# Kernel optimization log

Hardware: AMD Instinct MI355X
Metric: run time of the kernel (lower is better)

Reference implementation:

```python
import jax, jax.numpy as jnp
import numpy as np

N_NODES = 100000
N_EDGES = 1600000
F_IN = 256
HID = 256
N_CLS = 40


def _glorot(key, shape):
    lim = float(np.sqrt(6.0 / (shape[0] + shape[1])))
    return jax.random.uniform(key, shape, jnp.float32, -lim, lim)


def setup_inputs() -> dict:
    key = jax.random.key(0)
    ks = jax.random.split(key, 8)
    x = jax.random.normal(ks[0], (N_NODES, F_IN), jnp.float32)
    edge_index = jax.random.randint(ks[1], (2, N_EDGES), 0, N_NODES, jnp.int64)
    return {
        "x": x,
        "edge_index": edge_index,
        "W1": _glorot(ks[2], (F_IN, HID)),
        "b1": jnp.zeros((HID,), jnp.float32),
        "W2": _glorot(ks[3], (HID, HID)),
        "b2": jnp.zeros((HID,), jnp.float32),
        "W3": _glorot(ks[4], (HID, N_CLS)),
        "b3": jnp.zeros((N_CLS,), jnp.float32),
    }


def _gcn_conv(x, W, b, src, dst, norm, num_nodes):
    # linear transform first (PyG GCNConv), then normalized scatter-add
    h = x @ W                                   # [N, out]
    msg = h[src] * norm[:, None]                # [E+N, out] gathered messages
    out = jax.ops.segment_sum(msg, dst, num_segments=num_nodes)
    return out + b


def reference(x, edge_index, W1, b1, W2, b2, W3, b3):
    n = x.shape[0]
    loop = jnp.arange(n, dtype=edge_index.dtype)
    src = jnp.concatenate([edge_index[0], loop])  # add self-loops
    dst = jnp.concatenate([edge_index[1], loop])
    # symmetric GCN normalization: deg^{-1/2}[src] * deg^{-1/2}[dst]
    deg = jax.ops.segment_sum(jnp.ones_like(dst, dtype=x.dtype), dst, num_segments=n)
    dinv = jnp.where(deg > 0, jax.lax.rsqrt(deg), 0.0)
    norm = dinv[src] * dinv[dst]

    h = jax.nn.relu(_gcn_conv(x, W1, b1, src, dst, norm, n))  # dropout p=0.0 is identity
    h = jax.nn.relu(_gcn_conv(h, W2, b2, src, dst, norm, n))
    out = _gcn_conv(h, W3, b3, src, dst, norm, n)             # logits [N, num_classes]
    return out
```

## Files before the change

kernel.cpp:

```cpp
#include <hip/hip_runtime.h>
#include <hip/hip_bf16.h>
#include <cstdint>
#include <cstddef>

#define NNODES 100000
#define NEDGES 1600000
#define NCLS 40
#define NBLK_SCAN 391
#define NBUCK 391
#define BCAP 5120
#define NBLKB 256
#define CHUNK 6250
#define MPAD 100096

typedef _Float16 f16;
typedef _Float16 f16x8 __attribute__((ext_vector_type(8)));
typedef float f32x4 __attribute__((ext_vector_type(4)));

__device__ inline float h2f(unsigned short u) {
    f16 h; __builtin_memcpy(&h, &u, 2); return (float)h;
}
__device__ inline unsigned short f2h(float f) {
    f16 h = (f16)f; unsigned short u; __builtin_memcpy(&u, &h, 2); return u;
}
__device__ inline void gload_lds16(const void* g, void* l) {
    __builtin_amdgcn_global_load_lds((const __attribute__((address_space(1))) unsigned int*)g,
                                     (__attribute__((address_space(3))) unsigned int*)l, 16, 0, 0);
}
__device__ inline void fmix2(float& alo, float& ahi, unsigned u, float one) {
    asm("v_fma_mix_f32 %0, %1, %2, %0 op_sel:[0,0,0] op_sel_hi:[1,0,0]"
        : "+v"(alo) : "v"(u), "v"(one));
    asm("v_fma_mix_f32 %0, %1, %2, %0 op_sel:[1,0,0] op_sel_hi:[1,0,0]"
        : "+v"(ahi) : "v"(u), "v"(one));
}

__global__ void k_detect(const int* __restrict__ ei, int* __restrict__ flag) {
    if (threadIdx.x == 0 && blockIdx.x == 0) {
        int nz = 0;
        for (int i = 1; i < 256; i += 2) nz |= ei[i];
        *flag = (nz == 0) ? 1 : 0;
    }
}

__global__ __launch_bounds__(256) void k_bucket(const int* __restrict__ ei,
        const int* __restrict__ flag, int* __restrict__ gbcnt, int2* __restrict__ bedge) {
    __shared__ int lcnt[NBUCK], lbase[NBUCK], lcur[NBUCK];
    const int t = threadIdx.x;
    const int is64 = *flag;
    for (int i = t; i < NBUCK; i += 256) lcnt[i] = 0;
    __syncthreads();
    const int e0 = blockIdx.x * CHUNK;
    for (int i = t; i < CHUNK; i += 256) {
        int e = e0 + i;
        int d = is64 ? ei[2 * ((size_t)NEDGES + e)] : ei[NEDGES + e];
        atomicAdd(&lcnt[d >> 8], 1);
    }
    __syncthreads();
    for (int i = t; i < NBUCK; i += 256) {
        int c = lcnt[i];
        lbase[i] = c ? atomicAdd(&gbcnt[i], c) : 0;
        lcur[i] = 0;
    }
    __syncthreads();
    for (int i = t; i < CHUNK; i += 256) {
        int e = e0 + i;
        int s, d;
        if (is64) { s = ei[2 * (size_t)e]; d = ei[2 * ((size_t)NEDGES + e)]; }
        else      { s = ei[e];             d = ei[NEDGES + e]; }
        int b = d >> 8;
        int p = lbase[b] + atomicAdd(&lcur[b], 1);
        if (p < BCAP) bedge[(size_t)b * BCAP + p] = make_int2(s, d);
    }
}

__global__ __launch_bounds__(256) void k_cnt(const int* __restrict__ gbcnt,
        const int2* __restrict__ bedge, int* __restrict__ cnt) {
    __shared__ int lc[256];
    const int t = threadIdx.x, b = blockIdx.x;
    lc[t] = 0;
    __syncthreads();
    const int ne = min(gbcnt[b], BCAP);
    const int2* be = bedge + (size_t)b * BCAP;
    for (int i = t; i < ne; i += 256)
        atomicAdd(&lc[be[i].y & 255], 1);
    __syncthreads();
    int node = b * 256 + t;
    if (node < NNODES) cnt[node] = lc[t];
}

__global__ __launch_bounds__(256) void k_dinv(const int* __restrict__ cnt, float* __restrict__ dinv) {
    int i = blockIdx.x * 256 + threadIdx.x;
    if (i < MPAD) dinv[i] = (i < NNODES) ? rsqrtf((float)(cnt[i] + 1)) : 0.f;
}

__global__ __launch_bounds__(256) void k_scan1(const int* __restrict__ cnt,
        int* __restrict__ incl, int* __restrict__ blksum) {
    __shared__ int sm[256];
    const int t = threadIdx.x;
    int i = blockIdx.x * 256 + t;
    int v = (i < NNODES) ? (cnt[i] + 1) : 0;
    sm[t] = v;
    __syncthreads();
    for (int d = 1; d < 256; d <<= 1) {
        int x = (t >= d) ? sm[t - d] : 0;
        __syncthreads();
        sm[t] += x;
        __syncthreads();
    }
    if (i < NNODES) incl[i] = sm[t];
    if (t == 255) blksum[blockIdx.x] = sm[255];
}

__global__ __launch_bounds__(512) void k_scan2(const int* __restrict__ blksum, int* __restrict__ blkoff) {
    __shared__ int sm[512];
    const int t = threadIdx.x;
    int v = (t < NBLK_SCAN) ? blksum[t] : 0;
    sm[t] = v;
    __syncthreads();
    for (int d = 1; d < 512; d <<= 1) {
        int x = (t >= d) ? sm[t - d] : 0;
        __syncthreads();
        sm[t] += x;
        __syncthreads();
    }
    if (t < NBLK_SCAN) blkoff[t] = sm[t] - v;
}

__global__ __launch_bounds__(256) void k_scan3(const int* __restrict__ incl,
        const int* __restrict__ blkoff, int* __restrict__ offs) {
    int i = blockIdx.x * 256 + threadIdx.x;
    if (i < NNODES) offs[i + 1] = incl[i] + blkoff[blockIdx.x];
    if (i == 0) offs[0] = 0;
}

__global__ __launch_bounds__(256) void k_self(const int* __restrict__ offs, int* __restrict__ esrc) {
    int i = blockIdx.x * 256 + threadIdx.x;
    if (i < NNODES) esrc[offs[i]] = i;
}

__global__ __launch_bounds__(256) void k_fill2(const int* __restrict__ gbcnt,
        const int2* __restrict__ bedge, const int* __restrict__ offs, int* __restrict__ esrc) {
    __shared__ int loff[256], lcur[256];
    const int t = threadIdx.x, b = blockIdx.x;
    int node = b * 256 + t;
    loff[t] = (node < NNODES) ? offs[node] : 0;
    lcur[t] = 0;
    __syncthreads();
    const int ne = min(gbcnt[b], BCAP);
    const int2* be = bedge + (size_t)b * BCAP;
    for (int i = t; i < ne; i += 256) {
        int2 sd = be[i];
        int li = sd.y & 255;
        int p = loff[li] + 1 + atomicAdd(&lcur[li], 1);
        esrc[p] = sd.x;
    }
}

__global__ __launch_bounds__(256) void k_wt(const float* __restrict__ W, unsigned short* __restrict__ WT) {
    int k = blockIdx.x;
    int n = threadIdx.x;
    WT[n * 256 + k] = f2h(W[k * 256 + n]);
}

__global__ __launch_bounds__(256) void k_wt3(const float* __restrict__ W, unsigned short* __restrict__ WT) {
    int n = blockIdx.x;
    int k = threadIdx.x;
    WT[n * 256 + k] = (n < NCLS) ? f2h(W[k * NCLS + n]) : (unsigned short)0;
}

template<bool A32, bool NARROW>
__global__ __launch_bounds__(256) void gemm_core(const void* __restrict__ Ap,
        const unsigned short* __restrict__ BT, unsigned short* __restrict__ C,
        const float* __restrict__ dinv) {
    __shared__ __align__(16) char lds[65536];
    const int t = threadIdx.x;
    const int w = t >> 6, l = t & 63;
    const int bm = blockIdx.x * 128;
    const int bn = blockIdx.y * 128;
    const int lr = l >> 3, ls = l & 7;
    const unsigned short* A16 = (const unsigned short*)Ap;
    const float* A32p = (const float*)Ap;

    auto stageB = [&](int buf, int k0) {
        char* base = lds + buf * 32768 + 16384;
#pragma unroll
        for (int i = 0; i < 4; ++i) {
            int r = w * 32 + i * 8 + lr;
            int sl = ls ^ (r & 7);
            const char* gB = (const char*)BT + (size_t)(bn + r) * 512 + (size_t)k0 * 2 + sl * 16;
            gload_lds16(gB, base + (w * 32 + i * 8) * 128);
        }
    };
    auto stageA16 = [&](int buf, int k0) {
        char* base = lds + buf * 32768;
#pragma unroll
        for (int i = 0; i < 4; ++i) {
            int r = w * 32 + i * 8 + lr;
            int sl = ls ^ (r & 7);
            const char* gA = (const char*)A16 + (size_t)(bm + r) * 512 + (size_t)k0 * 2 + sl * 16;
            gload_lds16(gA, base + (w * 32 + i * 8) * 128);
        }
    };
    float4 areg[8];
    auto issueA32 = [&](int k0) {
#pragma unroll
        for (int i = 0; i < 8; ++i) {
            int tt = i * 256 + t;
            int r = tt >> 4, q = tt & 15;
            float4 v = make_float4(0.f, 0.f, 0.f, 0.f);
            if (bm + r < NNODES) v = *(const float4*)(A32p + (size_t)(bm + r) * 256 + k0 + q * 4);
            areg[i] = v;
        }
    };
    auto writeA32 = [&](int buf) {
        char* base = lds + buf * 32768;
#pragma unroll
        for (int i = 0; i < 8; ++i) {
            int tt = i * 256 + t;
            int r = tt >> 4, q = tt & 15;
            f16 h4[4] = {(f16)areg[i].x, (f16)areg[i].y, (f16)areg[i].z, (f16)areg[i].w};
            char* dst = base + r * 128 + (((q >> 1) ^ (r & 7)) * 16) + (q & 1) * 8;
            __builtin_memcpy(dst, h4, 8);
        }
    };

    f32x4 acc[4][4];
#pragma unroll
    for (int m = 0; m < 4; ++m)
#pragma unroll
        for (int n = 0; n < 4; ++n)
            acc[m][n] = (f32x4){0.f, 0.f, 0.f, 0.f};

    const int frow = l & 15, fk = l >> 4;
    const int r0w = (w >> 1) * 64, c0w = (w & 1) * 64;

    if constexpr (A32) { issueA32(0); } else { stageA16(0, 0); }
    stageB(0, 0);
    if constexpr (A32) { writeA32(0); }
    __syncthreads();
    for (int kt = 0; kt < 4; ++kt) {
        const int buf = kt & 1;
        if (kt < 3) {
            if constexpr (A32) { issueA32((kt + 1) * 64); } else { stageA16(buf ^ 1, (kt + 1) * 64); }
            stageB(buf ^ 1, (kt + 1) * 64);
        }
        const char* As = lds + buf * 32768;
        const char* Bs = As + 16384;
#pragma unroll
        for (int ks = 0; ks < 2; ++ks) {
            f16x8 af[4], bf[4];
#pragma unroll
            for (int m = 0; m < 4; ++m) {
                int ra = r0w + m * 16 + frow;
                af[m] = *(const f16x8*)(As + ra * 128 + (((ks * 4 + fk) ^ (ra & 7)) * 16));
            }
#pragma unroll
            for (int n = 0; n < 4; ++n) {
                int rb = c0w + n * 16 + frow;
                bf[n] = *(const f16x8*)(Bs + rb * 128 + (((ks * 4 + fk) ^ (rb & 7)) * 16));
            }
#pragma unroll
            for (int m = 0; m < 4; ++m)
#pragma unroll
                for (int n = 0; n < 4; ++n)
                    acc[m][n] = __builtin_amdgcn_mfma_f32_16x16x32_f16(af[m], bf[n], acc[m][n], 0, 0, 0);
        }
        if constexpr (A32) { if (kt < 3) writeA32(buf ^ 1); }
        __syncthreads();
    }

    unsigned short* Cs = (unsigned short*)lds;
    const int crow = (l >> 4) * 4, ccol = l & 15;
#pragma unroll
    for (int m = 0; m < 4; ++m) {
        float4 dv = *(const float4*)(dinv + bm + r0w + m * 16 + crow);
        float d4[4] = {dv.x, dv.y, dv.z, dv.w};
#pragma unroll
        for (int n = 0; n < 4; ++n)
#pragma unroll
            for (int r = 0; r < 4; ++r)
                Cs[(r0w + m * 16 + crow + r) * 136 + c0w + n * 16 + ccol] = f2h(acc[m][n][r] * d4[r]);
    }
    __syncthreads();
#pragma unroll
    for (int i = 0; i < 8; ++i) {
        int row = i * 16 + (t >> 4);
        int cs = t & 15;
        uint4 v = *(const uint4*)(Cs + row * 136 + cs * 8);
        if constexpr (NARROW) {
            if (cs < 5)
                *(uint4*)((char*)C + (size_t)(bm + row) * 80 + cs * 16) = v;
        } else {
            *(uint4*)((char*)C + (size_t)(bm + row) * 512 + bn * 2 + cs * 16) = v;
        }
    }
}

__global__ __launch_bounds__(256) void agg_v3(const unsigned short* __restrict__ T,
        const int* __restrict__ esrc, const int* __restrict__ offs,
        const float* __restrict__ dinv, const float* __restrict__ bias,
        unsigned short* __restrict__ outh) {
    int node = blockIdx.x * 4 + (threadIdx.x >> 6);
    if (node >= NNODES) return;
    const int l = threadIdx.x & 63;
    const float one = 1.0f;
    const int e0 = offs[node], e1 = offs[node + 1];
    const int ne = e1 - e0;
    const int myidx = esrc[e0 + min(l, ne - 1)];
    const char* Tb = (const char*)T;
    float a0 = 0.f, a1 = 0.f, a2 = 0.f, a3 = 0.f;
    const int nreg = min(ne, 64);
    int j = 0;
    for (; j + 8 <= nreg; j += 8) {
        uint2 u[8];
#pragma unroll
        for (int q = 0; q < 8; ++q) {
            int s = __builtin_amdgcn_readlane(myidx, j + q);
            u[q] = *(const uint2*)(Tb + (size_t)s * 512 + l * 8);
        }
#pragma unroll
        for (int q = 0; q < 8; ++q) {
            fmix2(a0, a1, u[q].x, one);
            fmix2(a2, a3, u[q].y, one);
        }
    }
    for (; j < nreg; ++j) {
        int s = __builtin_amdgcn_readlane(myidx, j);
        uint2 u = *(const uint2*)(Tb + (size_t)s * 512 + l * 8);
        fmix2(a0, a1, u.x, one);
        fmix2(a2, a3, u.y, one);
    }
    for (int e = e0 + 64; e < e1; ++e) {
        int s = esrc[e];
        uint2 u = *(const uint2*)(Tb + (size_t)s * 512 + l * 8);
        fmix2(a0, a1, u.x, one);
        fmix2(a2, a3, u.y, one);
    }
    float di = dinv[node];
    float4 bv = *(const float4*)(bias + l * 4);
    float r0 = fmaxf(fmaf(a0, di, bv.x), 0.f);
    float r1 = fmaxf(fmaf(a1, di, bv.y), 0.f);
    float r2 = fmaxf(fmaf(a2, di, bv.z), 0.f);
    float r3 = fmaxf(fmaf(a3, di, bv.w), 0.f);
    uint2 o;
    o.x = (unsigned)f2h(r0) | ((unsigned)f2h(r1) << 16);
    o.y = (unsigned)f2h(r2) | ((unsigned)f2h(r3) << 16);
    *(uint2*)(outh + (size_t)node * 256 + l * 4) = o;
}

__global__ __launch_bounds__(256) void agg_out_v3(const unsigned short* __restrict__ T,
        const int* __restrict__ esrc, const int* __restrict__ offs,
        const float* __restrict__ dinv, const float* __restrict__ bias,
        float* __restrict__ out) {
    int node = blockIdx.x * 4 + (threadIdx.x >> 6);
    if (node >= NNODES) return;
    const int l = threadIdx.x & 63;
    const int g = l >> 4, sl = l & 15;
    const bool act = sl < 10;
    const float one = 1.0f;
    const int e0 = offs[node], e1 = offs[node + 1];
    const int ne = e1 - e0;
    const int myidx = esrc[e0 + min(l, ne - 1)];
    const int nreg = min(ne, 64);
    const char* Tb = (const char*)T;
    float a0 = 0.f, a1 = 0.f, a2 = 0.f, a3 = 0.f;
    for (int j = 0; j < nreg; j += 4) {
        int jj = j + g;
        int s = __shfl(myidx, jj, 64);
        if (jj < nreg && act) {
            uint2 u = *(const uint2*)(Tb + (size_t)s * 80 + sl * 8);
            fmix2(a0, a1, u.x, one);
            fmix2(a2, a3, u.y, one);
        }
    }
    for (int e = e0 + 64 + g; e < e1; e += 4) {
        int s = esrc[e];
        if (act) {
            uint2 u = *(const uint2*)(Tb + (size_t)s * 80 + sl * 8);
            fmix2(a0, a1, u.x, one);
            fmix2(a2, a3, u.y, one);
        }
    }
    a0 += __shfl_xor(a0, 16, 64); a1 += __shfl_xor(a1, 16, 64);
    a2 += __shfl_xor(a2, 16, 64); a3 += __shfl_xor(a3, 16, 64);
    a0 += __shfl_xor(a0, 32, 64); a1 += __shfl_xor(a1, 32, 64);
    a2 += __shfl_xor(a2, 32, 64); a3 += __shfl_xor(a3, 32, 64);
    if (g == 0 && act) {
        float di = dinv[node];
        float4 bv = *(const float4*)(bias + sl * 4);
        float4 o = make_float4(fmaf(a0, di, bv.x), fmaf(a1, di, bv.y),
                               fmaf(a2, di, bv.z), fmaf(a3, di, bv.w));
        *(float4*)(out + (size_t)node * 40 + sl * 4) = o;
    }
}

extern "C" void kernel_launch(void* const* d_in, const int* in_sizes, int n_in,
                              void* d_out, int out_size, void* d_ws, size_t ws_size,
                              hipStream_t stream) {
    const float* x  = (const float*)d_in[0];
    const int*   ei = (const int*)d_in[1];
    const float* W1 = (const float*)d_in[2];
    const float* b1 = (const float*)d_in[3];
    const float* W2 = (const float*)d_in[4];
    const float* b2 = (const float*)d_in[5];
    const float* W3 = (const float*)d_in[6];
    const float* b3 = (const float*)d_in[7];
    float* out = (float*)d_out;

    char* ws = (char*)d_ws;
    size_t o = 0;
    unsigned short* tbA  = (unsigned short*)(ws + o); o += (size_t)MPAD * 256 * 2;
    unsigned short* tbB  = (unsigned short*)(ws + o); o += (size_t)MPAD * 256 * 2;
    unsigned short* tb40 = (unsigned short*)(ws + o); o += (size_t)MPAD * NCLS * 2;
    unsigned short* W1T  = (unsigned short*)(ws + o); o += 131072;
    unsigned short* W2T  = (unsigned short*)(ws + o); o += 131072;
    unsigned short* W3T  = (unsigned short*)(ws + o); o += 65536;
    int2* bedge  = (int2*)(ws + o);  o += (size_t)NBUCK * BCAP * 8;
    int* gbcnt   = (int*)(ws + o);   o += 2048;
    int* esrc    = (int*)(ws + o);   o += (size_t)(NEDGES + NNODES) * 4;
    int* cnt     = (int*)(ws + o);   o += 400128;
    int* offs    = (int*)(ws + o);   o += 400384;
    float* dinv  = (float*)(ws + o); o += 400384;
    int* incl    = (int*)(ws + o);   o += 400128;
    int* blksum  = (int*)(ws + o);   o += 2048;
    int* blkoff  = (int*)(ws + o);   o += 2048;
    int* flag    = (int*)(ws + o);   o += 256;
    if (ws_size < o) return;

    hipMemsetAsync(gbcnt, 0, 2048, stream);
    hipMemsetAsync(tbB + (size_t)NNODES * 256, 0, (MPAD - NNODES) * 512, stream);

    k_detect<<<1, 64, 0, stream>>>(ei, flag);
    k_bucket<<<NBLKB, 256, 0, stream>>>(ei, flag, gbcnt, bedge);
    k_cnt<<<NBUCK, 256, 0, stream>>>(gbcnt, bedge, cnt);
    k_dinv<<<(MPAD + 255) / 256, 256, 0, stream>>>(cnt, dinv);
    k_scan1<<<NBLK_SCAN, 256, 0, stream>>>(cnt, incl, blksum);
    k_scan2<<<1, 512, 0, stream>>>(blksum, blkoff);
    k_scan3<<<NBLK_SCAN, 256, 0, stream>>>(incl, blkoff, offs);
    k_self<<<NBLK_SCAN, 256, 0, stream>>>(offs, esrc);
    k_fill2<<<NBUCK, 256, 0, stream>>>(gbcnt, bedge, offs, esrc);

    k_wt<<<256, 256, 0, stream>>>(W1, W1T);
    k_wt<<<256, 256, 0, stream>>>(W2, W2T);
    k_wt3<<<128, 256, 0, stream>>>(W3, W3T);

    dim3 gg(MPAD / 128, 2), b256(256);
    gemm_core<true, false><<<gg, b256, 0, stream>>>(x, W1T, tbA, dinv);
    agg_v3<<<NNODES / 4, 256, 0, stream>>>(tbA, esrc, offs, dinv, b1, tbB);
    gemm_core<false, false><<<gg, b256, 0, stream>>>(tbB, W2T, tbA, dinv);
    agg_v3<<<NNODES / 4, 256, 0, stream>>>(tbA, esrc, offs, dinv, b2, tbB);
    gemm_core<false, true><<<dim3(MPAD / 128, 1), b256, 0, stream>>>(tbB, W3T, tb40, dinv);
    agg_out_v3<<<NNODES / 4, 256, 0, stream>>>(tb40, esrc, offs, dinv, b3, out);
}
```

Baseline: 492.2 us.

## Split hidden aggregation across feature quarters with four edge groups per wave

The 256-wide aggregation kernel now launches one block per (node-group, feature-quarter) pair. Each wave handles a 64-feature slice, with four 16-lane groups processing different edges in parallel and combining results through xor shuffles. Block indices are interleaved so that neighbouring blocks share the same quarter. The goal is more parallelism per node and more loads in flight on the irregular gather. In exchange, index loading and offset reads are repeated four times, the gathers are narrower, and the final reduction adds shuffle work.

```diff
diff --git a/kernel.cpp b/kernel.cpp
--- a/kernel.cpp
+++ b/kernel.cpp
@@ -296,56 +296,58 @@
     }
 }
 
-__global__ __launch_bounds__(256) void agg_v3(const unsigned short* __restrict__ T,
+__global__ __launch_bounds__(256) void agg_q2(const unsigned short* __restrict__ T,
         const int* __restrict__ esrc, const int* __restrict__ offs,
         const float* __restrict__ dinv, const float* __restrict__ bias,
         unsigned short* __restrict__ outh) {
-    int node = blockIdx.x * 4 + (threadIdx.x >> 6);
-    if (node >= NNODES) return;
+    const int n = blockIdx.x;
+    const int r = n & 7;
+    const int q = r >> 1;
+    const int c = ((n >> 3) << 1) + (r & 1);
+    const int node = c * 4 + (threadIdx.x >> 6);
     const int l = threadIdx.x & 63;
+    const int g = l >> 4, sl = l & 15;
     const float one = 1.0f;
     const int e0 = offs[node], e1 = offs[node + 1];
     const int ne = e1 - e0;
     const int myidx = esrc[e0 + min(l, ne - 1)];
-    const char* Tb = (const char*)T;
+    const int nreg = min(ne, 64);
+    const char* Tq = (const char*)T + q * 128;
     float a0 = 0.f, a1 = 0.f, a2 = 0.f, a3 = 0.f;
-    const int nreg = min(ne, 64);
-    int j = 0;
-    for (; j + 8 <= nreg; j += 8) {
-        uint2 u[8];
-#pragma unroll
-        for (int q = 0; q < 8; ++q) {
-            int s = __builtin_amdgcn_readlane(myidx, j + q);
-            u[q] = *(const uint2*)(Tb + (size_t)s * 512 + l * 8);
-        }
-#pragma unroll
-        for (int q = 0; q < 8; ++q) {
-            fmix2(a0, a1, u[q].x, one);
-            fmix2(a2, a3, u[q].y, one);
-        }
-    }
-    for (; j < nreg; ++j) {
-        int s = __builtin_amdgcn_readlane(myidx, j);
-        uint2 u = *(const uint2*)(Tb + (size_t)s * 512 + l * 8);
-        fmix2(a0, a1, u.x, one);
-        fmix2(a2, a3, u.y, one);
-    }
-    for (int e = e0 + 64; e < e1; ++e) {
+    for (int j = 0; j < nreg; j += 8) {
+        int j0 = j + g, j1 = j + g + 4;
+        int s0 = __shfl(myidx, min(j0, 63), 64);
+        int s1 = __shfl(myidx, min(j1, 63), 64);
+        if (j0 < nreg) {
+            uint2 u = *(const uint2*)(Tq + (size_t)s0 * 512 + sl * 8);
+            fmix2(a0, a1, u.x, one); fmix2(a2, a3, u.y, one);
+        }
+        if (j1 < nreg) {
+            uint2 u = *(const uint2*)(Tq + (size_t)s1 * 512 + sl * 8);
+            fmix2(a0, a1, u.x, one); fmix2(a2, a3, u.y, one);
+        }
+    }
+    for (int e = e0 + 64 + g; e < e1; e += 4) {
         int s = esrc[e];
-        uint2 u = *(const uint2*)(Tb + (size_t)s * 512 + l * 8);
-        fmix2(a0, a1, u.x, one);
-        fmix2(a2, a3, u.y, one);
-    }
-    float di = dinv[node];
-    float4 bv = *(const float4*)(bias + l * 4);
-    float r0 = fmaxf(fmaf(a0, di, bv.x), 0.f);
-    float r1 = fmaxf(fmaf(a1, di, bv.y), 0.f);
-    float r2 = fmaxf(fmaf(a2, di, bv.z), 0.f);
-    float r3 = fmaxf(fmaf(a3, di, bv.w), 0.f);
-    uint2 o;
-    o.x = (unsigned)f2h(r0) | ((unsigned)f2h(r1) << 16);
-    o.y = (unsigned)f2h(r2) | ((unsigned)f2h(r3) << 16);
-    *(uint2*)(outh + (size_t)node * 256 + l * 4) = o;
+        uint2 u = *(const uint2*)(Tq + (size_t)s * 512 + sl * 8);
+        fmix2(a0, a1, u.x, one); fmix2(a2, a3, u.y, one);
+    }
+    a0 += __shfl_xor(a0, 16, 64); a1 += __shfl_xor(a1, 16, 64);
+    a2 += __shfl_xor(a2, 16, 64); a3 += __shfl_xor(a3, 16, 64);
+    a0 += __shfl_xor(a0, 32, 64); a1 += __shfl_xor(a1, 32, 64);
+    a2 += __shfl_xor(a2, 32, 64); a3 += __shfl_xor(a3, 32, 64);
+    if (g == 0) {
+        float di = dinv[node];
+        float4 bv = *(const float4*)(bias + q * 64 + sl * 4);
+        float r0 = fmaxf(fmaf(a0, di, bv.x), 0.f);
+        float r1 = fmaxf(fmaf(a1, di, bv.y), 0.f);
+        float r2 = fmaxf(fmaf(a2, di, bv.z), 0.f);
+        float r3 = fmaxf(fmaf(a3, di, bv.w), 0.f);
+        uint2 o;
+        o.x = (unsigned)f2h(r0) | ((unsigned)f2h(r1) << 16);
+        o.y = (unsigned)f2h(r2) | ((unsigned)f2h(r3) << 16);
+        *(uint2*)(outh + (size_t)node * 256 + q * 64 + sl * 4) = o;
+    }
 }
 
 __global__ __launch_bounds__(256) void agg_out_v3(const unsigned short* __restrict__ T,
@@ -366,7 +368,7 @@
     float a0 = 0.f, a1 = 0.f, a2 = 0.f, a3 = 0.f;
     for (int j = 0; j < nreg; j += 4) {
         int jj = j + g;
-        int s = __shfl(myidx, jj, 64);
+        int s = __shfl(myidx, min(jj, 63), 64);
         if (jj < nreg && act) {
             uint2 u = *(const uint2*)(Tb + (size_t)s * 80 + sl * 8);
             fmix2(a0, a1, u.x, one);
@@ -446,9 +448,9 @@
 
     dim3 gg(MPAD / 128, 2), b256(256);
     gemm_core<true, false><<<gg, b256, 0, stream>>>(x, W1T, tbA, dinv);
-    agg_v3<<<NNODES / 4, 256, 0, stream>>>(tbA, esrc, offs, dinv, b1, tbB);
+    agg_q2<<<NNODES, 256, 0, stream>>>(tbA, esrc, offs, dinv, b1, tbB);
     gemm_core<false, false><<<gg, b256, 0, stream>>>(tbB, W2T, tbA, dinv);
-    agg_v3<<<NNODES / 4, 256, 0, stream>>>(tbA, esrc, offs, dinv, b2, tbB);
+    agg_q2<<<NNODES, 256, 0, stream>>>(tbA, esrc, offs, dinv, b2, tbB);
     gemm_core<false, true><<<dim3(MPAD / 128, 1), b256, 0, stream>>>(tbB, W3T, tb40, dinv);
     agg_out_v3<<<NNODES / 4, 256, 0, stream>>>(tb40, esrc, offs, dinv, b3, out);
 }
```

Result: slower. 616.5 us (+25.2%).
